# Performance work log

Hardware: AMD Instinct MI355X
Metric: run time of the kernel (lower is better)

Reference implementation:

```python
import jax, jax.numpy as jnp
import numpy as np

C = 0.01          # Poincare ball curvature 1/100
SQRT_C = 0.1
EPS = 1e-15
BALL_EPS = 4e-3   # geoopt float32 projx boundary epsilon


def _norm(x):
    return jnp.linalg.norm(x, axis=-1, keepdims=True)


def expmap0(u):
    n = jnp.maximum(_norm(u), EPS)
    return jnp.tanh(SQRT_C * n) * u / (SQRT_C * n)


def logmap0(x):
    n = jnp.maximum(_norm(x), EPS)
    t = jnp.clip(SQRT_C * n, -1.0 + 1e-7, 1.0 - 1e-7)
    return jnp.arctanh(t) * x / (SQRT_C * n)


def projx(x):
    maxnorm = (1.0 - BALL_EPS) / SQRT_C
    n = jnp.maximum(_norm(x), EPS)
    return jnp.where(n > maxnorm, x / n * maxnorm, x)


def mobius_matvec(M, x):
    xn = jnp.maximum(_norm(x), EPS)
    mx = x @ M.T
    mxn = jnp.maximum(_norm(mx), EPS)
    t = jnp.clip(SQRT_C * xn, -1.0 + 1e-7, 1.0 - 1e-7)
    res = jnp.tanh(mxn / xn * jnp.arctanh(t)) * mx / (mxn * SQRT_C)
    return jnp.where(jnp.all(mx == 0, axis=-1, keepdims=True), 0.0, res)


def mobius_add(x, y):
    x2 = jnp.sum(x * x, -1, keepdims=True)
    y2 = jnp.sum(y * y, -1, keepdims=True)
    xy = jnp.sum(x * y, -1, keepdims=True)
    num = (1 + 2 * C * xy + C * y2) * x + (1 - C * x2) * y
    den = 1 + 2 * C * xy + C * C * x2 * y2
    return num / jnp.maximum(den, EPS)


def hyp_linear(x, W, b):
    # eval mode: weight dropout is a no-op
    res = projx(mobius_matvec(W, x))
    hb = projx(expmap0(b.reshape(1, -1)))
    return projx(mobius_add(res, hb))


def setup_inputs() -> dict:
    key = jax.random.key(0)
    ks = jax.random.split(key, 10)
    B, S, N, H, HEADS, E = 2, 4, 10000, 64, 4, 160000
    G = B * S
    OC = H // HEADS
    # edges guaranteed to have no self-loops (module removes then re-adds them)
    src = jax.random.randint(ks[0], (G, E), 0, N)
    off = jax.random.randint(ks[1], (G, E), 1, N)
    dst = (src + off) % N
    edge_index = jnp.stack([src, dst], axis=1).astype(jnp.int32)  # [G,2,E]

    def glorot(k, shape, fan):
        a = np.sqrt(6.0 / fan)
        return jax.random.uniform(k, shape, minval=-a, maxval=a, dtype=jnp.float32)

    emb = jax.random.normal(ks[2], (N, H), dtype=jnp.float32)
    att_i = glorot(ks[3], (1, HEADS, OC), HEADS * OC + 1)
    att_j = glorot(ks[4], (1, HEADS, OC), HEADS * OC + 1)
    w1 = glorot(ks[5], (H, OC), H + OC)   # HypLinear(in=16, out=64): weight [out,in]
    b1 = jnp.zeros((H,), jnp.float32)
    w2 = glorot(ks[6], (H, H), H + H)
    b2 = jnp.zeros((H,), jnp.float32)
    history_graphs = jnp.zeros((B, S, N), jnp.float32)  # only shape is used
    return {"history_graphs": history_graphs, "edge_index": edge_index,
            "emb": emb, "att_i": att_i, "att_j": att_j,
            "w1": w1, "b1": b1, "w2": w2, "b2": b2}


def reference(history_graphs, edge_index, emb, att_i, att_j, w1, b1, w2, b2):
    B, S, N = history_graphs.shape
    G = edge_index.shape[0]
    H = emb.shape[1]
    heads = att_i.shape[1]
    oc = H // heads

    # node ids are arange(N) for every (b,s) -> identical features per graph
    x0 = projx(expmap0(emb))   # initHyperX, [N,H]
    xt = logmap0(x0)           # tangent features used by attention, [N,H]

    # add self loops (inputs contain none)
    loops = jnp.broadcast_to(jnp.arange(N, dtype=edge_index.dtype)[None, None, :], (G, 2, N))
    ei = jnp.concatenate([edge_index, loops], axis=-1)  # [G,2,E+N]

    def agg(e):
        src, dst = e[0], e[1]                       # targets (i), sources (j)
        x_i = xt[src].reshape(-1, heads, oc)        # [E2,h,oc]
        x_j = xt[dst].reshape(-1, heads, oc)
        alpha = jnp.sum(x_i * att_i, -1) + jnp.sum(x_j * att_j, -1)  # [E2,h]
        alpha = jax.nn.leaky_relu(alpha, 0.2)
        m = jax.ops.segment_max(alpha, src, num_segments=N)
        a = jnp.exp(alpha - m[src])
        s = jax.ops.segment_sum(a, src, num_segments=N)
        a = a / (s[src] + 1e-16)                    # edge softmax; dropout eval no-op
        sup = jax.ops.segment_sum(x_j * a[..., None], src, num_segments=N)  # [N,h,oc]
        sup = sup.mean(axis=1)                      # concat=False -> head mean, [N,oc]
        return projx(expmap0(sup))

    h = jax.vmap(agg)(ei)                           # [G,N,oc]
    node_emb = h.reshape(B, S, N, oc)[:, -1]        # last timestep, [B,N,oc]

    z = hyp_linear(node_emb, w1, b1)                # 16 -> 64
    z = projx(expmap0(jax.nn.silu(logmap0(z))))     # HypAct(SiLU)
    z = projx(expmap0(logmap0(z)))                  # HypDropout (eval: log/exp round trip)
    z = hyp_linear(z, w2, b2)                       # 64 -> 64
    return z
```

## Files before the change

### kernel.cpp

```cpp
#include <hip/hip_runtime.h>
#include <hip/hip_bf16.h>

#define N_NODES 10000
#define NE 160000
#define CAP 96
#define SQRT_C 0.1f
#define CC 0.01f
#define EPS 1e-15f
#define MAXNORM ((1.0f - 4e-3f) / SQRT_C)

__device__ __forceinline__ float fexp(float x) { return __expf(x); }
__device__ __forceinline__ float ftanh_pos(float x) {
    return 1.0f - 2.0f / (__expf(2.0f * x) + 1.0f);
}
__device__ __forceinline__ float fatanh01(float t) {
    return 0.5f * __logf((1.0f + t) / (1.0f - t));
}

__device__ __forceinline__ float ldf(const void* p, int i, int isbf) {
    return isbf ? __bfloat162float(((const __hip_bfloat16*)p)[i])
                : ((const float*)p)[i];
}

__device__ __forceinline__ int sniff_wave(const void* emb, int tid) {
    unsigned wv = ((const unsigned*)emb)[tid & 63];
    unsigned ex = (wv >> 7) & 0xFFu;
    unsigned long long m = __ballot(ex >= 116u && ex <= 133u);
    return (__popcll(m) >= 32) ? 1 : 0;
}

__device__ __forceinline__ float wsum(float v) {
#pragma unroll
    for (int off = 32; off > 0; off >>= 1) v += __shfl_xor(v, off, 64);
    return v;
}
__device__ __forceinline__ float wmax(float v) {
#pragma unroll
    for (int off = 32; off > 0; off >>= 1) v = fmaxf(v, __shfl_xor(v, off, 64));
    return v;
}

__global__ __launch_bounds__(256) void pre_scatter(const void* __restrict__ emb,
                                                   const void* __restrict__ att_i,
                                                   const void* __restrict__ att_j,
                                                   const void* __restrict__ w1g,
                                                   const void* __restrict__ b1g,
                                                   const void* __restrict__ w2g,
                                                   const void* __restrict__ b2g,
                                                   const int* __restrict__ ei,
                                                   float* __restrict__ xt,
                                                   float* __restrict__ ai,
                                                   float* __restrict__ aj,
                                                   int* __restrict__ cnt,
                                                   unsigned short* __restrict__ bucket,
                                                   int* __restrict__ ovf_cnt,
                                                   unsigned* __restrict__ ovf,
                                                   int* __restrict__ flag,
                                                   float* __restrict__ wf1t,
                                                   float* __restrict__ wf2t,
                                                   float* __restrict__ hb1f,
                                                   float* __restrict__ hb2f,
                                                   float* __restrict__ hbn2) {
    __shared__ int sflag;
    int tid = threadIdx.x;
    int w = tid >> 6, lane = tid & 63;
    if (blockIdx.x < 2500) {
        if (tid < 64) { int s = sniff_wave(emb, tid); if (tid == 0) sflag = s; }
        __syncthreads();
        int isbf = sflag;
        int t = blockIdx.x * 256 + tid;
        int node = t >> 6;
        float u = ldf(emb, node * 64 + lane, isbf);
        float n = fmaxf(sqrtf(wsum(u * u)), EPS);
        float th = ftanh_pos(SQRT_C * n);
        float x0 = th / (SQRT_C * n) * u;
        float x0n = th / SQRT_C;
        if (x0n > MAXNORM) { x0 *= MAXNORM / x0n; x0n = MAXNORM; }
        float tc = fminf(SQRT_C * x0n, 1.0f - 1e-7f);
        float xv = fatanh01(tc) / (SQRT_C * x0n) * x0;
        xt[node * 64 + lane] = xv;
        float pi = xv * ldf(att_i, lane, isbf);
        float pj = xv * ldf(att_j, lane, isbf);
#pragma unroll
        for (int off = 8; off > 0; off >>= 1) {
            pi += __shfl_xor(pi, off, 64);
            pj += __shfl_xor(pj, off, 64);
        }
        if ((lane & 15) == 0) {
            ai[node * 4 + (lane >> 4)] = pi;
            aj[node * 4 + (lane >> 4)] = pj;
        }
    } else if (blockIdx.x < 2813) {
        int e0 = (blockIdx.x - 2500) * 512 + tid;
#pragma unroll
        for (int q = 0; q < 2; ++q) {
            int e = e0 + q * 256;
            if (e >= NE) break;
            int s0 = ei[3 * 2 * NE + e], d0 = ei[3 * 2 * NE + NE + e];
            int s1 = ei[7 * 2 * NE + e], d1 = ei[7 * 2 * NE + NE + e];
            int i0 = s0, i1 = N_NODES + s1;
            int p0 = atomicAdd(&cnt[i0], 1);
            int p1 = atomicAdd(&cnt[i1], 1);
            if (p0 < CAP) bucket[i0 * CAP + p0] = (unsigned short)d0;
            else {
                int oi = atomicAdd(ovf_cnt, 1);
                ovf[oi] = (0u << 28) | ((unsigned)s0 << 14) | (unsigned)d0;
            }
            if (p1 < CAP) bucket[i1 * CAP + p1] = (unsigned short)d1;
            else {
                int oi = atomicAdd(ovf_cnt, 1);
                ovf[oi] = (1u << 28) | ((unsigned)s1 << 14) | (unsigned)d1;
            }
        }
    } else {
        if (tid < 64) { int s = sniff_wave(emb, tid); if (tid == 0) sflag = s; }
        __syncthreads();
        int isbf = sflag;
        if (tid == 0) *flag = isbf;
        for (int i = tid; i < 1024; i += 256) {
            int o = i >> 4, c = i & 15;
            wf1t[c * 64 + o] = ldf(w1g, i, isbf);
        }
        for (int i = tid; i < 4096; i += 256) {
            int o = i >> 6, c = i & 63;
            wf2t[c * 64 + o] = ldf(w2g, i, isbf);
        }
        if (w < 2) {
            const void* bg = w ? b2g : b1g;
            float b = ldf(bg, lane, isbf);
            float n = fmaxf(sqrtf(wsum(b * b)), EPS);
            float th = ftanh_pos(SQRT_C * n);
            float hv = th / (SQRT_C * n) * b;
            float hn = th / SQRT_C;
            if (hn > MAXNORM) { hv *= MAXNORM / hn; hn = MAXNORM; }
            (w ? hb2f : hb1f)[lane] = hv;
            if (lane == 0) hbn2[w] = hn * hn;
        }
    }
}

__global__ __launch_bounds__(256) void node_agg(const int* __restrict__ cnt,
                                                const unsigned short* __restrict__ bucket,
                                                const int* __restrict__ ovf_cnt,
                                                const unsigned* __restrict__ ovf,
                                                const float* __restrict__ ai,
                                                const float* __restrict__ aj,
                                                const float* __restrict__ xt,
                                                float* __restrict__ sup_t) {
    __shared__ float wlds[4][64 * 4];
    __shared__ int dlds[4][64];
    int w = threadIdx.x >> 6, lane = threadIdx.x & 63;
    int idx = blockIdx.x * 4 + w;
    int slot = (idx >= N_NODES) ? 1 : 0;
    int n = idx - slot * N_NODES;
    int deg = cnt[idx];
    int start = idx * CAP;

    float4 ai4 = *(const float4*)&ai[n * 4];
    float4 aj4n = *(const float4*)&aj[n * 4];
    float ain[4] = {ai4.x, ai4.y, ai4.z, ai4.w};
    float ajn[4] = {aj4n.x, aj4n.y, aj4n.z, aj4n.w};
    int hh = lane >> 4;
    float acc;

    if (deg <= 63) {
        bool act = (lane <= deg);
        int d = (lane < deg) ? (int)bucket[start + lane] : n;
        float4 a4 = act ? *(const float4*)&aj[d * 4] : make_float4(0.f, 0.f, 0.f, 0.f);
        float ajv[4] = {a4.x, a4.y, a4.z, a4.w};
        float eh[4];
#pragma unroll
        for (int h = 0; h < 4; ++h) {
            float a = ain[h] + ajv[h];
            a = (a < 0.0f) ? 0.2f * a : a;
            eh[h] = act ? fexp(a) : 0.0f;
        }
        float sh[4];
#pragma unroll
        for (int h = 0; h < 4; ++h) sh[h] = wsum(eh[h]);
#pragma unroll
        for (int h = 0; h < 4; ++h)
            wlds[w][lane * 4 + h] = eh[h] * (0.25f / (sh[h] + 1e-16f));
        dlds[w][lane] = d;
        int m = deg + 1;
        float s0 = 0.f, s1 = 0.f, s2 = 0.f, s3 = 0.f;
        float s4 = 0.f, s5 = 0.f, s6 = 0.f, s7 = 0.f;
        int e = 0;
        for (; e + 8 <= m; e += 8) {
            int d0 = dlds[w][e],     d1 = dlds[w][e + 1];
            int d2 = dlds[w][e + 2], d3 = dlds[w][e + 3];
            int d4 = dlds[w][e + 4], d5 = dlds[w][e + 5];
            int d6 = dlds[w][e + 6], d7 = dlds[w][e + 7];
            float w0 = wlds[w][(e + 0) * 4 + hh], w1 = wlds[w][(e + 1) * 4 + hh];
            float w2 = wlds[w][(e + 2) * 4 + hh], w3 = wlds[w][(e + 3) * 4 + hh];
            float w4 = wlds[w][(e + 4) * 4 + hh], w5 = wlds[w][(e + 5) * 4 + hh];
            float w6 = wlds[w][(e + 6) * 4 + hh], w7 = wlds[w][(e + 7) * 4 + hh];
            s0 = fmaf(w0, xt[d0 * 64 + lane], s0);
            s1 = fmaf(w1, xt[d1 * 64 + lane], s1);
            s2 = fmaf(w2, xt[d2 * 64 + lane], s2);
            s3 = fmaf(w3, xt[d3 * 64 + lane], s3);
            s4 = fmaf(w4, xt[d4 * 64 + lane], s4);
            s5 = fmaf(w5, xt[d5 * 64 + lane], s5);
            s6 = fmaf(w6, xt[d6 * 64 + lane], s6);
            s7 = fmaf(w7, xt[d7 * 64 + lane], s7);
        }
        for (; e + 4 <= m; e += 4) {
            int d0 = dlds[w][e],     d1 = dlds[w][e + 1];
            int d2 = dlds[w][e + 2], d3 = dlds[w][e + 3];
            float w0 = wlds[w][(e + 0) * 4 + hh], w1 = wlds[w][(e + 1) * 4 + hh];
            float w2 = wlds[w][(e + 2) * 4 + hh], w3 = wlds[w][(e + 3) * 4 + hh];
            s0 = fmaf(w0, xt[d0 * 64 + lane], s0);
            s1 = fmaf(w1, xt[d1 * 64 + lane], s1);
            s2 = fmaf(w2, xt[d2 * 64 + lane], s2);
            s3 = fmaf(w3, xt[d3 * 64 + lane], s3);
        }
        for (; e < m; ++e)
            s0 = fmaf(wlds[w][e * 4 + hh], xt[dlds[w][e] * 64 + lane], s0);
        acc = ((s0 + s1) + (s2 + s3)) + ((s4 + s5) + (s6 + s7));
    } else {
        int bdeg = (deg < CAP) ? deg : CAP;
        int tov = (deg > CAP) ? *ovf_cnt : 0;
        float mh[4];
#pragma unroll
        for (int h = 0; h < 4; ++h) {
            float a = ain[h] + ajn[h];
            mh[h] = (a < 0.0f) ? 0.2f * a : a;
        }
        for (int e = lane; e < bdeg; e += 64) {
            int d = bucket[start + e];
#pragma unroll
            for (int h = 0; h < 4; ++h) {
                float a = ain[h] + aj[d * 4 + h];
                a = (a < 0.0f) ? 0.2f * a : a;
                mh[h] = fmaxf(mh[h], a);
            }
        }
        for (int k = lane; k < tov; k += 64) {
            unsigned pe = ovf[k];
            if ((int)(pe >> 28) == slot && (int)((pe >> 14) & 0x3FFFu) == n) {
                int d = pe & 0x3FFFu;
#pragma unroll
                for (int h = 0; h < 4; ++h) {
                    float a = ain[h] + aj[d * 4 + h];
                    a = (a < 0.0f) ? 0.2f * a : a;
                    mh[h] = fmaxf(mh[h], a);
                }
            }
        }
#pragma unroll
        for (int h = 0; h < 4; ++h) mh[h] = wmax(mh[h]);
        float sh[4] = {0.f, 0.f, 0.f, 0.f};
        if (lane == 0) {
#pragma unroll
            for (int h = 0; h < 4; ++h) {
                float a = ain[h] + ajn[h];
                a = (a < 0.0f) ? 0.2f * a : a;
                sh[h] = fexp(a - mh[h]);
            }
        }
        for (int e = lane; e < bdeg; e += 64) {
            int d = bucket[start + e];
#pragma unroll
            for (int h = 0; h < 4; ++h) {
                float a = ain[h] + aj[d * 4 + h];
                a = (a < 0.0f) ? 0.2f * a : a;
                sh[h] += fexp(a - mh[h]);
            }
        }
        for (int k = lane; k < tov; k += 64) {
            unsigned pe = ovf[k];
            if ((int)(pe >> 28) == slot && (int)((pe >> 14) & 0x3FFFu) == n) {
                int d = pe & 0x3FFFu;
#pragma unroll
                for (int h = 0; h < 4; ++h) {
                    float a = ain[h] + aj[d * 4 + h];
                    a = (a < 0.0f) ? 0.2f * a : a;
                    sh[h] += fexp(a - mh[h]);
                }
            }
        }
#pragma unroll
        for (int h = 0; h < 4; ++h) sh[h] = wsum(sh[h]);
        float scale[4];
#pragma unroll
        for (int h = 0; h < 4; ++h) scale[h] = 0.25f / (sh[h] + 1e-16f);
        float aih = ain[hh], mhh = mh[hh], sch = scale[hh];
        float aself = aih + ajn[hh];
        aself = (aself < 0.0f) ? 0.2f * aself : aself;
        acc = fexp(aself - mhh) * sch * xt[n * 64 + lane];
        for (int e = 0; e < bdeg; ++e) {
            int d = bucket[start + e];
            float a = aih + aj[d * 4 + hh];
            a = (a < 0.0f) ? 0.2f * a : a;
            acc = fmaf(fexp(a - mhh) * sch, xt[d * 64 + lane], acc);
        }
        for (int k = 0; k < tov; ++k) {
            unsigned pe = ovf[k];
            if ((int)(pe >> 28) == slot && (int)((pe >> 14) & 0x3FFFu) == n) {
                int d = pe & 0x3FFFu;
                float a = aih + aj[d * 4 + hh];
                a = (a < 0.0f) ? 0.2f * a : a;
                acc = fmaf(fexp(a - mhh) * sch, xt[d * 64 + lane], acc);
            }
        }
    }
    acc += __shfl_xor(acc, 16, 64);
    acc += __shfl_xor(acc, 32, 64);
    if (lane < 16) sup_t[lane * 20000 + idx] = acc;
}

__global__ __launch_bounds__(256) void final_stage(const float* __restrict__ sup_t,
                                                   const float* __restrict__ wf1t,
                                                   const float* __restrict__ wf2t,
                                                   const float* __restrict__ hb1f,
                                                   const float* __restrict__ hb2f,
                                                   const float* __restrict__ hbn2,
                                                   const int* __restrict__ flag,
                                                   void* __restrict__ outv) {
    __shared__ float Z[65 * 64];
    __shared__ float pA[2][4][64];
    __shared__ float pB[2][4][64];
    int w = threadIdx.x >> 6, lane = threadIdx.x & 63;
    int base = blockIdx.x * 64;
    int nd = base + lane;
    bool valid = (nd < 2 * N_NODES);
    int isbf = *flag;
    float y2a = hbn2[0], y2b = hbn2[1];
    int ob = w * 16;

    float v[16];
#pragma unroll
    for (int c = 0; c < 16; ++c) v[c] = valid ? sup_t[c * 20000 + nd] : 0.0f;
    float n2 = 0.f;
#pragma unroll
    for (int c = 0; c < 16; ++c) n2 = fmaf(v[c], v[c], n2);
    float n = fmaxf(sqrtf(n2), EPS);
    float th0 = ftanh_pos(SQRT_C * n);
    float s0 = th0 / (SQRT_C * n);
    float x0n = th0 / SQRT_C;
    if (x0n > MAXNORM) { s0 *= MAXNORM / x0n; x0n = MAXNORM; }
#pragma unroll
    for (int c = 0; c < 16; ++c) v[c] *= s0;

    float a1[16];
#pragma unroll
    for (int oj = 0; oj < 16; ++oj) a1[oj] = 0.f;
#pragma unroll
    for (int c = 0; c < 16; ++c) {
        float vc = v[c];
#pragma unroll
        for (int oj = 0; oj < 16; ++oj)
            a1[oj] = fmaf(wf1t[c * 64 + ob + oj], vc, a1[oj]);
    }
    float pn = 0.f, ph = 0.f;
#pragma unroll
    for (int oj = 0; oj < 16; ++oj) {
        pn = fmaf(a1[oj], a1[oj], pn);
        ph = fmaf(a1[oj], hb1f[ob + oj], ph);
    }
    pA[0][w][lane] = pn; pA[1][w][lane] = ph;
    __syncthreads();
    float mxn2 = pA[0][0][lane] + pA[0][1][lane] + pA[0][2][lane] + pA[0][3][lane];
    float mxhb = pA[1][0][lane] + pA[1][1][lane] + pA[1][2][lane] + pA[1][3][lane];

    float z2n;
    {
        float xn = fmaxf(x0n, EPS);
        float mxn = fmaxf(sqrtf(mxn2), EPS);
        float t = fminf(SQRT_C * xn, 1.0f - 1e-7f);
        float th = ftanh_pos(mxn / xn * fatanh01(t));
        float rs = th / (mxn * SQRT_C);
        float rn = th / SQRT_C;
        if (mxn2 == 0.0f) { rs = 0.f; rn = 0.f; }
        if (rn > MAXNORM) { rs *= MAXNORM / rn; rn = MAXNORM; }
        float xy = rs * mxhb;
        float x2 = rn * rn;
        float A = 1.0f + 2.0f * CC * xy + CC * y2a;
        float B = 1.0f - CC * x2;
        float rden = 1.0f / fmaxf(1.0f + 2.0f * CC * xy + CC * CC * x2 * y2a, EPS);
        float pz = 0.f;
#pragma unroll
        for (int oj = 0; oj < 16; ++oj) {
            float z = (A * rs * a1[oj] + B * hb1f[ob + oj]) * rden;
            a1[oj] = z;
            pz = fmaf(z, z, pz);
        }
        pB[0][w][lane] = pz;
        __syncthreads();
        float zn2 = pB[0][0][lane] + pB[0][1][lane] + pB[0][2][lane] + pB[0][3][lane];
        float zn = fmaxf(sqrtf(zn2), EPS);
        float sc = (zn > MAXNORM) ? MAXNORM / zn : 1.0f;
        float z1n = fminf(zn, MAXNORM);
        float lg = fatanh01(fminf(SQRT_C * z1n, 1.0f - 1e-7f)) / (SQRT_C * z1n) * sc;
        float pu = 0.f;
#pragma unroll
        for (int oj = 0; oj < 16; ++oj) {
            float u = lg * a1[oj];
            u = u / (1.0f + __expf(-u));
            a1[oj] = u;
            pu = fmaf(u, u, pu);
        }
        pA[0][w][lane] = pu;
        __syncthreads();
        float un2 = pA[0][0][lane] + pA[0][1][lane] + pA[0][2][lane] + pA[0][3][lane];
        float un = fmaxf(sqrtf(un2), EPS);
        float th2 = ftanh_pos(SQRT_C * un);
        float s2 = th2 / (SQRT_C * un);
        z2n = th2 / SQRT_C;
        if (z2n > MAXNORM) { s2 *= MAXNORM / z2n; z2n = MAXNORM; }
#pragma unroll
        for (int oj = 0; oj < 16; ++oj) Z[(ob + oj) * 64 + lane] = a1[oj] * s2;
    }
    __syncthreads();

    float a2[16];
#pragma unroll
    for (int oj = 0; oj < 16; ++oj) a2[oj] = 0.f;
#pragma unroll 4
    for (int c = 0; c < 64; ++c) {
        float zc = Z[c * 64 + lane];
#pragma unroll
        for (int oj = 0; oj < 16; ++oj)
            a2[oj] = fmaf(wf2t[c * 64 + ob + oj], zc, a2[oj]);
    }
    float pn2 = 0.f, ph2 = 0.f;
#pragma unroll
    for (int oj = 0; oj < 16; ++oj) {
        pn2 = fmaf(a2[oj], a2[oj], pn2);
        ph2 = fmaf(a2[oj], hb2f[ob + oj], ph2);
    }
    pB[0][w][lane] = pn2; pB[1][w][lane] = ph2;
    __syncthreads();
    float mxn2b = pB[0][0][lane] + pB[0][1][lane] + pB[0][2][lane] + pB[0][3][lane];
    float mxhb2 = pB[1][0][lane] + pB[1][1][lane] + pB[1][2][lane] + pB[1][3][lane];
    {
        float xn = fmaxf(z2n, EPS);
        float mxn = fmaxf(sqrtf(mxn2b), EPS);
        float t = fminf(SQRT_C * xn, 1.0f - 1e-7f);
        float th = ftanh_pos(mxn / xn * fatanh01(t));
        float rs = th / (mxn * SQRT_C);
        float rn = th / SQRT_C;
        if (mxn2b == 0.0f) { rs = 0.f; rn = 0.f; }
        if (rn > MAXNORM) { rs *= MAXNORM / rn; rn = MAXNORM; }
        float xy = rs * mxhb2;
        float x2 = rn * rn;
        float A = 1.0f + 2.0f * CC * xy + CC * y2b;
        float B = 1.0f - CC * x2;
        float rden = 1.0f / fmaxf(1.0f + 2.0f * CC * xy + CC * CC * x2 * y2b, EPS);
        float pz = 0.f;
#pragma unroll
        for (int oj = 0; oj < 16; ++oj) {
            float z = (A * rs * a2[oj] + B * hb2f[ob + oj]) * rden;
            a2[oj] = z;
            pz = fmaf(z, z, pz);
        }
        pA[0][w][lane] = pz;
        __syncthreads();
        float zn2 = pA[0][0][lane] + pA[0][1][lane] + pA[0][2][lane] + pA[0][3][lane];
        float zn = fmaxf(sqrtf(zn2), EPS);
        float s4 = (zn > MAXNORM) ? MAXNORM / zn : 1.0f;
#pragma unroll
        for (int oj = 0; oj < 16; ++oj) Z[(ob + oj) * 65 + lane] = a2[oj] * s4;
    }
    __syncthreads();

#pragma unroll 1
    for (int k = 0; k < 16; ++k) {
        int nl = w * 16 + k;
        int ng = base + nl;
        if (ng >= 2 * N_NODES) break;
        float val = Z[lane * 65 + nl];
        if (isbf) ((__hip_bfloat16*)outv)[ng * 64 + lane] = __float2bfloat16(val);
        else      ((float*)outv)[ng * 64 + lane] = val;
    }
}

extern "C" void kernel_launch(void* const* d_in, const int* in_sizes, int n_in,
                              void* d_out, int out_size, void* d_ws, size_t ws_size,
                              hipStream_t stream) {
    const int* ei = (const int*)d_in[1];
    const void* emb   = d_in[2];
    const void* att_i = d_in[3];
    const void* att_j = d_in[4];
    const void* w1 = d_in[5];
    const void* b1 = d_in[6];
    const void* w2 = d_in[7];
    const void* b2 = d_in[8];

    float* ws = (float*)d_ws;
    float* xt    = ws;
    float* ai    = ws + 640000;
    float* aj    = ws + 680000;
    float* sup_t = ws + 720000;
    int* cnt     = (int*)(ws + 1040000);
    int* ovf_cnt = (int*)(ws + 1060000);
    unsigned short* bucket = (unsigned short*)(ws + 1060032);
    unsigned* ovf = (unsigned*)(ws + 2020032);
    int* flag     = (int*)(ws + 2340032);
    float* wf1t = ws + 2340064;
    float* wf2t = ws + 2341088;
    float* hb1f = ws + 2345184;
    float* hb2f = ws + 2345248;
    float* hbn2 = ws + 2345312;

    hipMemsetAsync((void*)cnt, 0, (2 * N_NODES + 8) * sizeof(int), stream);
    hipLaunchKernelGGL(pre_scatter, dim3(2814), dim3(256), 0, stream,
                       emb, att_i, att_j, w1, b1, w2, b2, ei,
                       xt, ai, aj, cnt, bucket, ovf_cnt, ovf, flag,
                       wf1t, wf2t, hb1f, hb2f, hbn2);
    hipLaunchKernelGGL(node_agg, dim3(5000), dim3(256), 0, stream,
                       cnt, bucket, ovf_cnt, ovf, ai, aj, xt, sup_t);
    hipLaunchKernelGGL(final_stage, dim3(313), dim3(256), 0, stream,
                       sup_t, wf1t, wf2t, hb1f, hb2f, hbn2, flag, d_out);
}
```

Measured before the change: 142.2 us.

## Restructure final stage to one wave per node with shuffle reductions

The final stage now assigns one 64-lane wave per node, with each lane owning one output channel. Norm and dot-product reductions use wave shuffles (wsum) instead of shared-memory partials and block barriers, and W2 is staged transposed in shared memory. The sup_t layout changes to node-major so each node's 16 features are contiguous. The grid grows to 1250 blocks that each process 16 nodes, which removes the repeated __syncthreads but adds many shuffles per node and reloads the weights in every block.

```diff
diff --git a/kernel.cpp b/kernel.cpp
--- a/kernel.cpp
+++ b/kernel.cpp
@@ -306,7 +306,7 @@
     }
     acc += __shfl_xor(acc, 16, 64);
     acc += __shfl_xor(acc, 32, 64);
-    if (lane < 16) sup_t[lane * 20000 + idx] = acc;
+    if (lane < 16) sup_t[idx * 16 + lane] = acc;
 }
 
 __global__ __launch_bounds__(256) void final_stage(const float* __restrict__ sup_t,
@@ -317,54 +317,39 @@
                                                    const float* __restrict__ hbn2,
                                                    const int* __restrict__ flag,
                                                    void* __restrict__ outv) {
-    __shared__ float Z[65 * 64];
-    __shared__ float pA[2][4][64];
-    __shared__ float pB[2][4][64];
-    int w = threadIdx.x >> 6, lane = threadIdx.x & 63;
-    int base = blockIdx.x * 64;
-    int nd = base + lane;
-    bool valid = (nd < 2 * N_NODES);
+    __shared__ float w2s[64][68];
+    int tid = threadIdx.x, w = tid >> 6, lane = tid & 63;
+    for (int i = tid; i < 4096; i += 256) {
+        int c = i >> 6, o = i & 63;
+        w2s[o][c] = wf2t[i];
+    }
+    float w1r[16];
+#pragma unroll
+    for (int c = 0; c < 16; ++c) w1r[c] = wf1t[c * 64 + lane];
+    float hb1 = hb1f[lane], hb2v = hb2f[lane];
+    float y2a = hbn2[0], y2b = hbn2[1];
     int isbf = *flag;
-    float y2a = hbn2[0], y2b = hbn2[1];
-    int ob = w * 16;
-
-    float v[16];
-#pragma unroll
-    for (int c = 0; c < 16; ++c) v[c] = valid ? sup_t[c * 20000 + nd] : 0.0f;
-    float n2 = 0.f;
-#pragma unroll
-    for (int c = 0; c < 16; ++c) n2 = fmaf(v[c], v[c], n2);
-    float n = fmaxf(sqrtf(n2), EPS);
-    float th0 = ftanh_pos(SQRT_C * n);
-    float s0 = th0 / (SQRT_C * n);
-    float x0n = th0 / SQRT_C;
-    if (x0n > MAXNORM) { s0 *= MAXNORM / x0n; x0n = MAXNORM; }
-#pragma unroll
-    for (int c = 0; c < 16; ++c) v[c] *= s0;
-
-    float a1[16];
-#pragma unroll
-    for (int oj = 0; oj < 16; ++oj) a1[oj] = 0.f;
-#pragma unroll
-    for (int c = 0; c < 16; ++c) {
-        float vc = v[c];
-#pragma unroll
-        for (int oj = 0; oj < 16; ++oj)
-            a1[oj] = fmaf(wf1t[c * 64 + ob + oj], vc, a1[oj]);
-    }
-    float pn = 0.f, ph = 0.f;
-#pragma unroll
-    for (int oj = 0; oj < 16; ++oj) {
-        pn = fmaf(a1[oj], a1[oj], pn);
-        ph = fmaf(a1[oj], hb1f[ob + oj], ph);
-    }
-    pA[0][w][lane] = pn; pA[1][w][lane] = ph;
     __syncthreads();
-    float mxn2 = pA[0][0][lane] + pA[0][1][lane] + pA[0][2][lane] + pA[0][3][lane];
-    float mxhb = pA[1][0][lane] + pA[1][1][lane] + pA[1][2][lane] + pA[1][3][lane];
-
-    float z2n;
-    {
+
+#pragma unroll 1
+    for (int k = 0; k < 4; ++k) {
+        int nd = blockIdx.x * 4 + w + k * 5000;
+        float vl = (lane < 16) ? sup_t[nd * 16 + lane] : 0.0f;
+        float n2 = wsum(vl * vl);
+        float n = fmaxf(sqrtf(n2), EPS);
+        float th0 = ftanh_pos(SQRT_C * n);
+        float s0 = th0 / (SQRT_C * n);
+        float x0n = th0 / SQRT_C;
+        if (x0n > MAXNORM) { s0 *= MAXNORM / x0n; x0n = MAXNORM; }
+
+        float a1 = 0.f;
+#pragma unroll
+        for (int c = 0; c < 16; ++c)
+            a1 = fmaf(w1r[c], __shfl(vl, c, 64), a1);
+        a1 *= s0;
+
+        float mxn2 = wsum(a1 * a1);
+        float mxhb = wsum(a1 * hb1);
         float xn = fmaxf(x0n, EPS);
         float mxn = fmaxf(sqrtf(mxn2), EPS);
         float t = fminf(SQRT_C * xn, 1.0f - 1e-7f);
@@ -378,100 +363,56 @@
         float A = 1.0f + 2.0f * CC * xy + CC * y2a;
         float B = 1.0f - CC * x2;
         float rden = 1.0f / fmaxf(1.0f + 2.0f * CC * xy + CC * CC * x2 * y2a, EPS);
-        float pz = 0.f;
-#pragma unroll
-        for (int oj = 0; oj < 16; ++oj) {
-            float z = (A * rs * a1[oj] + B * hb1f[ob + oj]) * rden;
-            a1[oj] = z;
-            pz = fmaf(z, z, pz);
-        }
-        pB[0][w][lane] = pz;
-        __syncthreads();
-        float zn2 = pB[0][0][lane] + pB[0][1][lane] + pB[0][2][lane] + pB[0][3][lane];
+        float z = (A * rs * a1 + B * hb1) * rden;
+
+        float zn2 = wsum(z * z);
         float zn = fmaxf(sqrtf(zn2), EPS);
         float sc = (zn > MAXNORM) ? MAXNORM / zn : 1.0f;
         float z1n = fminf(zn, MAXNORM);
         float lg = fatanh01(fminf(SQRT_C * z1n, 1.0f - 1e-7f)) / (SQRT_C * z1n) * sc;
-        float pu = 0.f;
-#pragma unroll
-        for (int oj = 0; oj < 16; ++oj) {
-            float u = lg * a1[oj];
-            u = u / (1.0f + __expf(-u));
-            a1[oj] = u;
-            pu = fmaf(u, u, pu);
-        }
-        pA[0][w][lane] = pu;
-        __syncthreads();
-        float un2 = pA[0][0][lane] + pA[0][1][lane] + pA[0][2][lane] + pA[0][3][lane];
+        float u = lg * z;
+        u = u / (1.0f + __expf(-u));
+        float un2 = wsum(u * u);
         float un = fmaxf(sqrtf(un2), EPS);
         float th2 = ftanh_pos(SQRT_C * un);
         float s2 = th2 / (SQRT_C * un);
-        z2n = th2 / SQRT_C;
+        float z2n = th2 / SQRT_C;
         if (z2n > MAXNORM) { s2 *= MAXNORM / z2n; z2n = MAXNORM; }
-#pragma unroll
-        for (int oj = 0; oj < 16; ++oj) Z[(ob + oj) * 64 + lane] = a1[oj] * s2;
-    }
-    __syncthreads();
-
-    float a2[16];
-#pragma unroll
-    for (int oj = 0; oj < 16; ++oj) a2[oj] = 0.f;
-#pragma unroll 4
-    for (int c = 0; c < 64; ++c) {
-        float zc = Z[c * 64 + lane];
-#pragma unroll
-        for (int oj = 0; oj < 16; ++oj)
-            a2[oj] = fmaf(wf2t[c * 64 + ob + oj], zc, a2[oj]);
-    }
-    float pn2 = 0.f, ph2 = 0.f;
-#pragma unroll
-    for (int oj = 0; oj < 16; ++oj) {
-        pn2 = fmaf(a2[oj], a2[oj], pn2);
-        ph2 = fmaf(a2[oj], hb2f[ob + oj], ph2);
-    }
-    pB[0][w][lane] = pn2; pB[1][w][lane] = ph2;
-    __syncthreads();
-    float mxn2b = pB[0][0][lane] + pB[0][1][lane] + pB[0][2][lane] + pB[0][3][lane];
-    float mxhb2 = pB[1][0][lane] + pB[1][1][lane] + pB[1][2][lane] + pB[1][3][lane];
-    {
-        float xn = fmaxf(z2n, EPS);
-        float mxn = fmaxf(sqrtf(mxn2b), EPS);
-        float t = fminf(SQRT_C * xn, 1.0f - 1e-7f);
-        float th = ftanh_pos(mxn / xn * fatanh01(t));
-        float rs = th / (mxn * SQRT_C);
-        float rn = th / SQRT_C;
-        if (mxn2b == 0.0f) { rs = 0.f; rn = 0.f; }
-        if (rn > MAXNORM) { rs *= MAXNORM / rn; rn = MAXNORM; }
-        float xy = rs * mxhb2;
-        float x2 = rn * rn;
-        float A = 1.0f + 2.0f * CC * xy + CC * y2b;
-        float B = 1.0f - CC * x2;
-        float rden = 1.0f / fmaxf(1.0f + 2.0f * CC * xy + CC * CC * x2 * y2b, EPS);
-        float pz = 0.f;
-#pragma unroll
-        for (int oj = 0; oj < 16; ++oj) {
-            float z = (A * rs * a2[oj] + B * hb2f[ob + oj]) * rden;
-            a2[oj] = z;
-            pz = fmaf(z, z, pz);
-        }
-        pA[0][w][lane] = pz;
-        __syncthreads();
-        float zn2 = pA[0][0][lane] + pA[0][1][lane] + pA[0][2][lane] + pA[0][3][lane];
-        float zn = fmaxf(sqrtf(zn2), EPS);
-        float s4 = (zn > MAXNORM) ? MAXNORM / zn : 1.0f;
-#pragma unroll
-        for (int oj = 0; oj < 16; ++oj) Z[(ob + oj) * 65 + lane] = a2[oj] * s4;
-    }
-    __syncthreads();
-
-#pragma unroll 1
-    for (int k = 0; k < 16; ++k) {
-        int nl = w * 16 + k;
-        int ng = base + nl;
-        if (ng >= 2 * N_NODES) break;
-        float val = Z[lane * 65 + nl];
-        if (isbf) ((__hip_bfloat16*)outv)[ng * 64 + lane] = __float2bfloat16(val);
-        else      ((float*)outv)[ng * 64 + lane] = val;
+        float z2 = u * s2;
+
+        float a2 = 0.f;
+#pragma unroll
+        for (int j = 0; j < 16; ++j) {
+            const float4 wq = *(const float4*)&w2s[lane][j * 4];
+            a2 = fmaf(wq.x, __shfl(z2, 4 * j + 0, 64), a2);
+            a2 = fmaf(wq.y, __shfl(z2, 4 * j + 1, 64), a2);
+            a2 = fmaf(wq.z, __shfl(z2, 4 * j + 2, 64), a2);
+            a2 = fmaf(wq.w, __shfl(z2, 4 * j + 3, 64), a2);
+        }
+
+        float pn2 = wsum(a2 * a2);
+        float ph2 = wsum(a2 * hb2v);
+        float xnb = fmaxf(z2n, EPS);
+        float mxnb = fmaxf(sqrtf(pn2), EPS);
+        float tb = fminf(SQRT_C * xnb, 1.0f - 1e-7f);
+        float thb = ftanh_pos(mxnb / xnb * fatanh01(tb));
+        float rsb = thb / (mxnb * SQRT_C);
+        float rnb = thb / SQRT_C;
+        if (pn2 == 0.0f) { rsb = 0.f; rnb = 0.f; }
+        if (rnb > MAXNORM) { rsb *= MAXNORM / rnb; rnb = MAXNORM; }
+        float xyb = rsb * ph2;
+        float x2b = rnb * rnb;
+        float Ab = 1.0f + 2.0f * CC * xyb + CC * y2b;
+        float Bb = 1.0f - CC * x2b;
+        float rdenb = 1.0f / fmaxf(1.0f + 2.0f * CC * xyb + CC * CC * x2b * y2b, EPS);
+        float zf = (Ab * rsb * a2 + Bb * hb2v) * rdenb;
+        float zf2 = wsum(zf * zf);
+        float znf = fmaxf(sqrtf(zf2), EPS);
+        float s4 = (znf > MAXNORM) ? MAXNORM / znf : 1.0f;
+        float val = zf * s4;
+
+        if (isbf) ((__hip_bfloat16*)outv)[nd * 64 + lane] = __float2bfloat16(val);
+        else      ((float*)outv)[nd * 64 + lane] = val;
     }
 }
 
@@ -510,6 +451,6 @@
                        wf1t, wf2t, hb1f, hb2f, hbn2);
     hipLaunchKernelGGL(node_agg, dim3(5000), dim3(256), 0, stream,
                        cnt, bucket, ovf_cnt, ovf, ai, aj, xt, sup_t);
-    hipLaunchKernelGGL(final_stage, dim3(313), dim3(256), 0, stream,
+    hipLaunchKernelGGL(final_stage, dim3(1250), dim3(256), 0, stream,
                        sup_t, wf1t, wf2t, hb1f, hb2f, hbn2, flag, d_out);
 }
```

After: 161.4 us. 13.5% more time.
